# Optimization experiments

Measured on AMD Instinct MI355X. Metric: run time of the kernel, lower is better.

## Reference

```python
import jax, jax.numpy as jnp
import numpy as np

HEADS = 8

def setup_inputs() -> dict:
    key = jax.random.key(0)
    ks = jax.random.split(key, 4)
    b, n, d = 4, 4097, 128  # n = 64*64 + 1 (CLS + spatial)
    x = jax.random.normal(ks[0], (b, n, d), dtype=jnp.float32)
    W_qkv = jax.random.normal(ks[1], (d, 3 * d), dtype=jnp.float32) * (d ** -0.5)
    b_qkv = jnp.zeros((3 * d,), dtype=jnp.float32)
    W_out = jax.random.normal(ks[2], (d, d), dtype=jnp.float32) * (d ** -0.5)
    b_out = jnp.zeros((d,), dtype=jnp.float32)
    return {"x": x, "W_qkv": W_qkv, "b_qkv": b_qkv, "W_out": W_out, "b_out": b_out}

def reference(x, W_qkv, b_qkv, W_out, b_out):
    b, n, d = x.shape
    h = HEADS
    dh = d // h
    scale = d ** -0.5  # note: module scales by dim**-0.5, not head_dim**-0.5
    qkv = x @ W_qkv + b_qkv                      # [b, n, 3d]
    q, k, v = jnp.split(qkv, 3, axis=-1)
    def to_heads(t):
        return t.reshape(b, n, h, dh).transpose(0, 2, 1, 3)  # [b, h, n, dh]
    q, k, v = to_heads(q), to_heads(k), to_heads(v)
    dots = jnp.einsum('bhid,bhjd->bhij', q, k) * scale       # [b, h, n, n]
    attn = jax.nn.softmax(dots, axis=-1)
    out = jnp.einsum('bhij,bhjd->bhid', attn, v)             # [b, h, n, dh]
    out = out.transpose(0, 2, 1, 3).reshape(b, n, d)
    return out @ W_out + b_out
```

## Files before the change

### kernel.cpp

```cpp
#include <hip/hip_runtime.h>
#include <hip/hip_bf16.h>
#include <stdint.h>


#define BB 4
#define NN 4097
#define NNP 4112
#define DD 128
#define HH 8
#define DH 16
#define BH (BB*HH)
#define ROWS (BB*NN)
#define MT  1025

typedef _Float16 h4 __attribute__((ext_vector_type(4)));
typedef _Float16 h8 __attribute__((ext_vector_type(8)));
typedef __fp16   fp16v2 __attribute__((ext_vector_type(2)));
typedef float    f4 __attribute__((ext_vector_type(4)));

#define QSCALE (0.08838834764831845f * 1.4426950408889634f)

#if __has_builtin(__builtin_amdgcn_exp2f)
#define EXP2F(x) __builtin_amdgcn_exp2f(x)
#else
#define EXP2F(x) exp2f(x)
#endif

union H4u { h4 v; fp16v2 p[2]; };
union H8u { h8 v; fp16v2 p[4]; };

static __device__ __forceinline__ H4u pack4u(float a, float b, float c, float d) {
    H4u u;
#if __has_builtin(__builtin_amdgcn_cvt_pkrtz)
    u.p[0] = __builtin_amdgcn_cvt_pkrtz(a, b);
    u.p[1] = __builtin_amdgcn_cvt_pkrtz(c, d);
#else
    u.v[0] = (_Float16)a; u.v[1] = (_Float16)b; u.v[2] = (_Float16)c; u.v[3] = (_Float16)d;
#endif
    return u;
}

__global__ __launch_bounds__(256) void prep(
    const float* __restrict__ x,
    const float* __restrict__ Wqkv,
    const float* __restrict__ Wout,
    _Float16* __restrict__ x16,
    _Float16* __restrict__ WqkvT,
    _Float16* __restrict__ WoutT)
{
    const int id = blockIdx.x*256 + threadIdx.x;
    const int NX8 = ROWS*DD/8;
    if (id < NX8) {
        const float4* s = (const float4*)(x + (size_t)id*8);
        const float4 a = s[0], b = s[1];
        const H4u u0 = pack4u(a.x, a.y, a.z, a.w);
        const H4u u1 = pack4u(b.x, b.y, b.z, b.w);
        h4* d = (h4*)(x16 + (size_t)id*8);
        d[0] = u0.v; d[1] = u1.v;
    } else if (id < NX8 + 384*128) {
        const int e = id - NX8;
        const int n = e >> 7, k = e & 127;
        const float s = (n < 128) ? QSCALE : 1.0f;
        WqkvT[e] = (_Float16)(Wqkv[k*384 + n] * s);
    } else if (id < NX8 + 384*128 + 128*128) {
        const int e = id - NX8 - 384*128;
        const int n = e >> 7, k = e & 127;
        WoutT[e] = (_Float16)(Wout[k*128 + n]);
    }
}

__global__ __launch_bounds__(256) void qkv_mfma(
    const _Float16* __restrict__ x16,
    const _Float16* __restrict__ WqkvT,
    const float* __restrict__ bqkv,
    _Float16* __restrict__ Qh,
    _Float16* __restrict__ Kh,
    _Float16* __restrict__ Vh)
{
    const int wid  = blockIdx.x;
    const int wave = threadIdx.x >> 6;
    const int lane = threadIdx.x & 63;
    const int quad = lane >> 4, l16 = lane & 15;

    const int arow = wid*16 + l16;
    const int arc  = (arow < ROWS) ? arow : (ROWS - 1);
    h8 af[4];
    #pragma unroll
    for (int kk = 0; kk < 4; ++kk)
        af[kk] = *(const h8*)(x16 + (size_t)arc*DD + kk*32 + quad*8);

    const int r0 = wid*16 + quad*4;
    const int nt0 = wave*6;

    for (int nt = nt0; nt < nt0 + 6; nt += 2) {
        const float b0 = bqkv[nt*16 + l16]      * ((nt   < 8) ? QSCALE : 1.0f);
        const float b1 = bqkv[nt*16 + 16 + l16] * ((nt+1 < 8) ? QSCALE : 1.0f);
        f4 a0 = {b0,b0,b0,b0}, a1 = {b1,b1,b1,b1};
        #pragma unroll
        for (int kk = 0; kk < 4; ++kk) {
            const h8 bf0 = *(const h8*)(WqkvT + (size_t)(nt*16      + l16)*DD + kk*32 + quad*8);
            const h8 bf1 = *(const h8*)(WqkvT + (size_t)(nt*16 + 16 + l16)*DD + kk*32 + quad*8);
            a0 = __builtin_amdgcn_mfma_f32_16x16x32_f16(af[kk], bf0, a0, 0, 0, 0);
            a1 = __builtin_amdgcn_mfma_f32_16x16x32_f16(af[kk], bf1, a1, 0, 0, 0);
        }
        #pragma unroll
        for (int u = 0; u < 2; ++u) {
            const int ntc = nt + u;
            const int which = ntc >> 3, head = ntc & 7;
            _Float16* base = (which == 0) ? Qh : ((which == 1) ? Kh : Vh);
            const f4 av = u ? a1 : a0;
            #pragma unroll
            for (int r = 0; r < 4; ++r) {
                const int row = r0 + r;
                if (row < ROWS) {
                    const int bidx = row / NN;
                    const int nrow = row - bidx*NN;
                    base[((size_t)(bidx*HH + head)*NNP + nrow)*DH + l16] = (_Float16)av[r];
                }
            }
        }
    }
}

__global__ __launch_bounds__(256) void vt_transpose(
    const _Float16* __restrict__ Vh,
    _Float16* __restrict__ Vt)
{
    __shared__ _Float16 tile[128][DH + 2];
    const int tl  = blockIdx.x;
    const int bh  = blockIdx.y;
    const int tid = threadIdx.x;
    const int n0  = tl * 128;
    const int rem = (n0 + 128 <= NNP) ? 128 : (NNP - n0);

    {
        const int r  = tid >> 1;
        const int i8 = (tid & 1) * 8;
        const int rc = (r < rem) ? r : (rem - 1);
        const h8 v = *(const h8*)(Vh + ((size_t)bh*NNP + n0 + rc)*DH + i8);
        #pragma unroll
        for (int j = 0; j < 8; ++j) tile[r][i8 + j] = v[j];
    }
    __syncthreads();
    {
        const int i    = tid >> 4;
        const int nseg = tid & 15;
        if (nseg * 8 < rem) {
            h8 v;
            #pragma unroll
            for (int j = 0; j < 8; ++j) v[j] = tile[nseg*8 + j][i];
            *(h8*)(Vt + ((size_t)bh*DH + i)*NNP + n0 + nseg*8) = v;
        }
    }
}

__global__ __launch_bounds__(128, 6) void attn_mfma(
    const _Float16* __restrict__ Qh,
    const _Float16* __restrict__ Kh,
    const _Float16* __restrict__ Vt,
    _Float16* __restrict__ PACC,
    float* __restrict__ PL)
{
    const int qc2  = blockIdx.x;
    const int bh   = blockIdx.y;
    const int sp   = blockIdx.z;
    const int tid  = threadIdx.x;
    const int wave = tid >> 6;
    const int lane = tid & 63;
    const int quad = lane >> 4;
    const int l16  = lane & 15;
    const int bidx = bh >> 3, head = bh & 7;

    const int qbase = (qc2*2 + wave)*64;

    const _Float16* Qb = Qh + (size_t)bh*NNP*DH;
    h8 qf[4];
    #pragma unroll
    for (int g = 0; g < 4; ++g) {
        h8 t = {0,0,0,0,0,0,0,0};
        if (quad < 2) {
            const int qr = qbase + g*16 + l16;
            const int qc = (qr < NN) ? qr : (NN-1);
            t = *(const h8*)(Qb + (size_t)qc*DH + quad*8);
        }
        qf[g] = t;
    }

    f4 acc[4] = {{0,0,0,0},{0,0,0,0},{0,0,0,0},{0,0,0,0}};
    float ls[4] = {0.f,0.f,0.f,0.f};

    const int t0 = sp*64;
    const int t1 = t0 + 64;

    const _Float16* kp = Kh + ((size_t)bh*NNP + (size_t)t0*16 + l16)*DH + (quad&1)*8;
    const _Float16* vp = Vt + ((size_t)bh*DH + l16)*NNP + t0*16 + quad*4;

    h8 ak = *(const h8*)kp;
    h4 av = *(const h4*)vp;
    const f4 zero = {0.f,0.f,0.f,0.f};
#if __has_builtin(__builtin_amdgcn_fdot2)
    const fp16v2 one2 = {(__fp16)1.0f, (__fp16)1.0f};
#endif

    for (int tt = t0; tt < t1; ++tt) {
        kp += 16*DH; vp += 16;
        const h8 nak = *(const h8*)kp;
        const h4 nav = *(const h4*)vp;
        #pragma unroll
        for (int g = 0; g < 4; ++g) {
            f4 d = __builtin_amdgcn_mfma_f32_16x16x32_f16(ak, qf[g], zero, 0, 0, 0);
            const float p0 = EXP2F(d[0]), p1 = EXP2F(d[1]), p2 = EXP2F(d[2]), p3 = EXP2F(d[3]);
            const H4u pb = pack4u(p0, p1, p2, p3);
#if __has_builtin(__builtin_amdgcn_fdot2)
            ls[g] = __builtin_amdgcn_fdot2(pb.p[0], one2,
                     __builtin_amdgcn_fdot2(pb.p[1], one2, ls[g], false), false);
#else
            ls[g] += (p0 + p1) + (p2 + p3);
#endif
            acc[g] = __builtin_amdgcn_mfma_f32_16x16x16f16(av, pb.v, acc[g], 0, 0, 0);
        }
        ak = nak; av = nav;
    }

    if (sp == 3) {
        #pragma unroll
        for (int g = 0; g < 4; ++g) {
            f4 d = __builtin_amdgcn_mfma_f32_16x16x32_f16(ak, qf[g], zero, 0, 0, 0);
            const float p0 = (quad == 0) ? EXP2F(d[0]) : 0.f;
            ls[g] += p0;
            const H4u pb = pack4u(p0, 0.f, 0.f, 0.f);
            acc[g] = __builtin_amdgcn_mfma_f32_16x16x16f16(av, pb.v, acc[g], 0, 0, 0);
        }
    }

    const size_t rb = (size_t)sp*ROWS + (size_t)bidx*NN;
    #pragma unroll
    for (int g = 0; g < 4; ++g) {
        float l = ls[g];
        l += __shfl_xor(l, 16);
        l += __shfl_xor(l, 32);
        const int qr = qbase + g*16 + l16;
        if (qr < NN) {
            const float inv = 1.0f / l;
            const H4u st = pack4u(acc[g][0]*inv, acc[g][1]*inv, acc[g][2]*inv, acc[g][3]*inv);
            *(h4*)(PACC + (rb + qr)*DD + head*DH + quad*4) = st.v;
            if (quad == 0) PL[(rb + qr)*HH + head] = l;
        }
    }
}

__global__ __launch_bounds__(256) void out_mfma(
    const _Float16* __restrict__ PACC,
    const float* __restrict__ PL,
    const _Float16* __restrict__ WoutT,
    const float* __restrict__ bout,
    float* __restrict__ out)
{
    const int wid  = blockIdx.x*4 + (threadIdx.x >> 6);
    if (wid >= MT) return;
    const int lane = threadIdx.x & 63;
    const int quad = lane >> 4, l16 = lane & 15;
    const int hq   = quad >> 1;

    const int arow = wid*16 + l16;
    const int arc  = (arow < ROWS) ? arow : (ROWS - 1);

    h8 af[4];
    #pragma unroll
    for (int kk = 0; kk < 4; ++kk) {
        const int head = kk*2 + hq;
        float n0=0.f,n1=0.f,n2=0.f,n3=0.f,n4=0.f,n5=0.f,n6=0.f,n7=0.f,lsum=0.f;
        #pragma unroll
        for (int sp = 0; sp < 4; ++sp) {
            const float l = PL[((size_t)sp*ROWS + arc)*HH + head];
            lsum += l;
            const h8 p = *(const h8*)(PACC + ((size_t)sp*ROWS + arc)*DD + kk*32 + quad*8);
            n0 += l*(float)p[0]; n1 += l*(float)p[1];
            n2 += l*(float)p[2]; n3 += l*(float)p[3];
            n4 += l*(float)p[4]; n5 += l*(float)p[5];
            n6 += l*(float)p[6]; n7 += l*(float)p[7];
        }
        const float inv = 1.0f / lsum;
        H8u u;
#if __has_builtin(__builtin_amdgcn_cvt_pkrtz)
        u.p[0] = __builtin_amdgcn_cvt_pkrtz(n0*inv, n1*inv);
        u.p[1] = __builtin_amdgcn_cvt_pkrtz(n2*inv, n3*inv);
        u.p[2] = __builtin_amdgcn_cvt_pkrtz(n4*inv, n5*inv);
        u.p[3] = __builtin_amdgcn_cvt_pkrtz(n6*inv, n7*inv);
#else
        u.v[0]=(_Float16)(n0*inv); u.v[1]=(_Float16)(n1*inv);
        u.v[2]=(_Float16)(n2*inv); u.v[3]=(_Float16)(n3*inv);
        u.v[4]=(_Float16)(n4*inv); u.v[5]=(_Float16)(n5*inv);
        u.v[6]=(_Float16)(n6*inv); u.v[7]=(_Float16)(n7*inv);
#endif
        af[kk] = u.v;
    }

    const int r0 = wid*16 + quad*4;

    for (int nt = 0; nt < 8; nt += 2) {
        const float b0 = bout[nt*16 + l16];
        const float b1 = bout[nt*16 + 16 + l16];
        f4 a0 = {b0,b0,b0,b0}, a1 = {b1,b1,b1,b1};
        #pragma unroll
        for (int kk = 0; kk < 4; ++kk) {
            const h8 bf0 = *(const h8*)(WoutT + (size_t)(nt*16      + l16)*DD + kk*32 + quad*8);
            const h8 bf1 = *(const h8*)(WoutT + (size_t)(nt*16 + 16 + l16)*DD + kk*32 + quad*8);
            a0 = __builtin_amdgcn_mfma_f32_16x16x32_f16(af[kk], bf0, a0, 0, 0, 0);
            a1 = __builtin_amdgcn_mfma_f32_16x16x32_f16(af[kk], bf1, a1, 0, 0, 0);
        }
        #pragma unroll
        for (int r = 0; r < 4; ++r) {
            const int row = r0 + r;
            if (row < ROWS) {
                out[(size_t)row*DD + nt*16      + l16] = a0[r];
                out[(size_t)row*DD + nt*16 + 16 + l16] = a1[r];
            }
        }
    }
}

extern "C" void kernel_launch(void* const* d_in, const int* in_sizes, int n_in,
                              void* d_out, int out_size, void* d_ws, size_t ws_size,
                              hipStream_t stream) {
    const float* x    = (const float*)d_in[0];
    const float* Wqkv = (const float*)d_in[1];
    const float* bqkv = (const float*)d_in[2];
    const float* Wout = (const float*)d_in[3];
    const float* bout = (const float*)d_in[4];
    for (int i = 0; i < n_in; ++i) {
        switch (in_sizes[i]) {
            case 2097664: x    = (const float*)d_in[i]; break;
            case 49152:   Wqkv = (const float*)d_in[i]; break;
            case 384:     bqkv = (const float*)d_in[i]; break;
            case 16384:   Wout = (const float*)d_in[i]; break;
            case 128:     bout = (const float*)d_in[i]; break;
            default: break;
        }
    }
    float* out = (float*)d_out;

    const size_t perh = (size_t)BH * NNP * DH;
    _Float16* Qh   = (_Float16*)d_ws;
    _Float16* Kh   = Qh + perh;
    _Float16* Vt   = Kh + perh;
    _Float16* Vh   = Vt + perh;
    _Float16* PACC = Vh;
    _Float16* x16  = Vh + perh;
    float*    PL    = (float*)(PACC + (size_t)4*ROWS*DD);
    _Float16* WqkvT = (_Float16*)(PL + (size_t)4*ROWS*HH);
    _Float16* WoutT = WqkvT + 384*128;

    const int NX8 = ROWS*DD/8;
    const int prep_total = NX8 + 384*128 + 128*128;

    hipLaunchKernelGGL(prep, dim3((prep_total + 255)/256), dim3(256), 0, stream,
                       x, Wqkv, Wout, x16, WqkvT, WoutT);
    hipLaunchKernelGGL(qkv_mfma, dim3(MT), dim3(256), 0, stream,
                       x16, WqkvT, bqkv, Qh, Kh, Vh);
    hipLaunchKernelGGL(vt_transpose, dim3(33, BH), dim3(256), 0, stream,
                       Vh, Vt);
    hipLaunchKernelGGL(attn_mfma, dim3(33, BH, 4), dim3(128), 0, stream,
                       Qh, Kh, Vt, PACC, PL);
    hipLaunchKernelGGL(out_mfma, dim3((MT + 3)/4), dim3(256), 0, stream,
                       PACC, PL, WoutT, bout, out);
}
```

Measured before the change: 188.2 us.

## Halve KV splits, use 256-thread attention blocks with 16x16x16 QK MFMA

The attention kernel now splits the key range into two chunks instead of four and uses 256-thread blocks covering 256 query rows, with the launch grid adjusted to match. The QK product switches from a zero-padded 16x16x32 MFMA to a 16x16x16 MFMA with h4 fragments. The key loop is unrolled by two. The output kernel preloads all partial results and the whole W_out fragment set into registers before merging the two splits. The aim is to cut the partial-result write and merge traffic and remove the wasted half of the QK MFMA, at the cost of fewer total blocks for load balancing and more register pressure in out_mfma.

```diff
diff --git a/kernel.cpp b/kernel.cpp
--- a/kernel.cpp
+++ b/kernel.cpp
@@ -12,6 +12,7 @@
 #define BH (BB*HH)
 #define ROWS (BB*NN)
 #define MT  1025
+#define NSP 2
 
 typedef _Float16 h4 __attribute__((ext_vector_type(4)));
 typedef _Float16 h8 __attribute__((ext_vector_type(8)));
@@ -154,14 +155,14 @@
     }
 }
 
-__global__ __launch_bounds__(128, 6) void attn_mfma(
+__global__ __launch_bounds__(256, 8) void attn_mfma(
     const _Float16* __restrict__ Qh,
     const _Float16* __restrict__ Kh,
     const _Float16* __restrict__ Vt,
     _Float16* __restrict__ PACC,
     float* __restrict__ PL)
 {
-    const int qc2  = blockIdx.x;
+    const int qt   = blockIdx.x;
     const int bh   = blockIdx.y;
     const int sp   = blockIdx.z;
     const int tid  = threadIdx.x;
@@ -171,44 +172,41 @@
     const int l16  = lane & 15;
     const int bidx = bh >> 3, head = bh & 7;
 
-    const int qbase = (qc2*2 + wave)*64;
+    const int qbase = qt*256 + wave*64;
 
     const _Float16* Qb = Qh + (size_t)bh*NNP*DH;
-    h8 qf[4];
+    h4 qf[4];
     #pragma unroll
     for (int g = 0; g < 4; ++g) {
-        h8 t = {0,0,0,0,0,0,0,0};
-        if (quad < 2) {
-            const int qr = qbase + g*16 + l16;
-            const int qc = (qr < NN) ? qr : (NN-1);
-            t = *(const h8*)(Qb + (size_t)qc*DH + quad*8);
-        }
-        qf[g] = t;
+        const int qr = qbase + g*16 + l16;
+        const int qc = (qr < NN) ? qr : (NN-1);
+        qf[g] = *(const h4*)(Qb + (size_t)qc*DH + quad*4);
     }
 
     f4 acc[4] = {{0,0,0,0},{0,0,0,0},{0,0,0,0},{0,0,0,0}};
     float ls[4] = {0.f,0.f,0.f,0.f};
 
-    const int t0 = sp*64;
-    const int t1 = t0 + 64;
-
-    const _Float16* kp = Kh + ((size_t)bh*NNP + (size_t)t0*16 + l16)*DH + (quad&1)*8;
+    const int t0 = sp*(4096/NSP/16);
+    const int t1 = t0 + (4096/NSP/16);
+
+    const _Float16* kp = Kh + ((size_t)bh*NNP + (size_t)t0*16 + l16)*DH + quad*4;
     const _Float16* vp = Vt + ((size_t)bh*DH + l16)*NNP + t0*16 + quad*4;
 
-    h8 ak = *(const h8*)kp;
+    h4 ak = *(const h4*)kp;
     h4 av = *(const h4*)vp;
     const f4 zero = {0.f,0.f,0.f,0.f};
 #if __has_builtin(__builtin_amdgcn_fdot2)
     const fp16v2 one2 = {(__fp16)1.0f, (__fp16)1.0f};
 #endif
 
+    #pragma unroll 2
     for (int tt = t0; tt < t1; ++tt) {
         kp += 16*DH; vp += 16;
-        const h8 nak = *(const h8*)kp;
+        const h4 nak = *(const h4*)kp;
         const h4 nav = *(const h4*)vp;
         #pragma unroll
         for (int g = 0; g < 4; ++g) {
-            f4 d = __builtin_amdgcn_mfma_f32_16x16x32_f16(ak, qf[g], zero, 0, 0, 0);
+            f4 d = __builtin_amdgcn_mfma_f32_16x16x16f16(ak, qf[g], zero, 0, 0, 0);
             const float p0 = EXP2F(d[0]), p1 = EXP2F(d[1]), p2 = EXP2F(d[2]), p3 = EXP2F(d[3]);
             const H4u pb = pack4u(p0, p1, p2, p3);
 #if __has_builtin(__builtin_amdgcn_fdot2)
@@ -222,10 +220,10 @@
         ak = nak; av = nav;
     }
 
-    if (sp == 3) {
+    if (sp == NSP-1) {
         #pragma unroll
         for (int g = 0; g < 4; ++g) {
-            f4 d = __builtin_amdgcn_mfma_f32_16x16x32_f16(ak, qf[g], zero, 0, 0, 0);
+            f4 d = __builtin_amdgcn_mfma_f32_16x16x16f16(ak, qf[g], zero, 0, 0, 0);
             const float p0 = (quad == 0) ? EXP2F(d[0]) : 0.f;
             ls[g] += p0;
             const H4u pb = pack4u(p0, 0.f, 0.f, 0.f);
@@ -249,7 +247,7 @@
     }
 }
 
-__global__ __launch_bounds__(256) void out_mfma(
+__global__ __launch_bounds__(256, 1) void out_mfma(
     const _Float16* __restrict__ PACC,
     const float* __restrict__ PL,
     const _Float16* __restrict__ WoutT,
@@ -265,49 +263,58 @@
     const int arow = wid*16 + l16;
     const int arc  = (arow < ROWS) ? arow : (ROWS - 1);
 
+    h8 pf[NSP][4]; float lv[NSP][4];
+    #pragma unroll
+    for (int sp = 0; sp < NSP; ++sp) {
+        const _Float16* pb  = PACC + ((size_t)sp*ROWS + arc)*DD;
+        const float*    plb = PL   + ((size_t)sp*ROWS + arc)*HH;
+        #pragma unroll
+        for (int kk = 0; kk < 4; ++kk) {
+            pf[sp][kk] = *(const h8*)(pb + kk*32 + quad*8);
+            lv[sp][kk] = plb[kk*2 + hq];
+        }
+    }
+    h8 wf[4][2][4];
+    #pragma unroll
+    for (int p = 0; p < 4; ++p)
+        #pragma unroll
+        for (int u = 0; u < 2; ++u)
+            #pragma unroll
+            for (int kk = 0; kk < 4; ++kk)
+                wf[p][u][kk] = *(const h8*)(WoutT + (size_t)((p*2+u)*16 + l16)*DD + kk*32 + quad*8);
+
     h8 af[4];
     #pragma unroll
     for (int kk = 0; kk < 4; ++kk) {
-        const int head = kk*2 + hq;
-        float n0=0.f,n1=0.f,n2=0.f,n3=0.f,n4=0.f,n5=0.f,n6=0.f,n7=0.f,lsum=0.f;
-        #pragma unroll
-        for (int sp = 0; sp < 4; ++sp) {
-            const float l = PL[((size_t)sp*ROWS + arc)*HH + head];
-            lsum += l;
-            const h8 p = *(const h8*)(PACC + ((size_t)sp*ROWS + arc)*DD + kk*32 + quad*8);
-            n0 += l*(float)p[0]; n1 += l*(float)p[1];
-            n2 += l*(float)p[2]; n3 += l*(float)p[3];
-            n4 += l*(float)p[4]; n5 += l*(float)p[5];
-            n6 += l*(float)p[6]; n7 += l*(float)p[7];
-        }
-        const float inv = 1.0f / lsum;
+        const float l0 = lv[0][kk], l1 = lv[1][kk];
+        const float inv = 1.0f / (l0 + l1);
+        const float s0 = l0*inv, s1 = l1*inv;
         H8u u;
+        #pragma unroll
+        for (int j = 0; j < 4; ++j) {
+            const float a = s0*(float)pf[0][kk][2*j]   + s1*(float)pf[1][kk][2*j];
+            const float b = s0*(float)pf[0][kk][2*j+1] + s1*(float)pf[1][kk][2*j+1];
 #if __has_builtin(__builtin_amdgcn_cvt_pkrtz)
-        u.p[0] = __builtin_amdgcn_cvt_pkrtz(n0*inv, n1*inv);
-        u.p[1] = __builtin_amdgcn_cvt_pkrtz(n2*inv, n3*inv);
-        u.p[2] = __builtin_amdgcn_cvt_pkrtz(n4*inv, n5*inv);
-        u.p[3] = __builtin_amdgcn_cvt_pkrtz(n6*inv, n7*inv);
+            u.p[j] = __builtin_amdgcn_cvt_pkrtz(a, b);
 #else
-        u.v[0]=(_Float16)(n0*inv); u.v[1]=(_Float16)(n1*inv);
-        u.v[2]=(_Float16)(n2*inv); u.v[3]=(_Float16)(n3*inv);
-        u.v[4]=(_Float16)(n4*inv); u.v[5]=(_Float16)(n5*inv);
-        u.v[6]=(_Float16)(n6*inv); u.v[7]=(_Float16)(n7*inv);
-#endif
+            u.v[2*j] = (_Float16)a; u.v[2*j+1] = (_Float16)b;
+#endif
+        }
         af[kk] = u.v;
     }
 
     const int r0 = wid*16 + quad*4;
 
-    for (int nt = 0; nt < 8; nt += 2) {
+    #pragma unroll
+    for (int p = 0; p < 4; ++p) {
+        const int nt = p*2;
         const float b0 = bout[nt*16 + l16];
         const float b1 = bout[nt*16 + 16 + l16];
         f4 a0 = {b0,b0,b0,b0}, a1 = {b1,b1,b1,b1};
         #pragma unroll
         for (int kk = 0; kk < 4; ++kk) {
-            const h8 bf0 = *(const h8*)(WoutT + (size_t)(nt*16      + l16)*DD + kk*32 + quad*8);
-            const h8 bf1 = *(const h8*)(WoutT + (size_t)(nt*16 + 16 + l16)*DD + kk*32 + quad*8);
-            a0 = __builtin_amdgcn_mfma_f32_16x16x32_f16(af[kk], bf0, a0, 0, 0, 0);
-            a1 = __builtin_amdgcn_mfma_f32_16x16x32_f16(af[kk], bf1, a1, 0, 0, 0);
+            a0 = __builtin_amdgcn_mfma_f32_16x16x32_f16(af[kk], wf[p][0][kk], a0, 0, 0, 0);
+            a1 = __builtin_amdgcn_mfma_f32_16x16x32_f16(af[kk], wf[p][1][kk], a1, 0, 0, 0);
         }
         #pragma unroll
         for (int r = 0; r < 4; ++r) {
@@ -347,8 +354,8 @@
     _Float16* Vh   = Vt + perh;
     _Float16* PACC = Vh;
     _Float16* x16  = Vh + perh;
-    float*    PL    = (float*)(PACC + (size_t)4*ROWS*DD);
-    _Float16* WqkvT = (_Float16*)(PL + (size_t)4*ROWS*HH);
+    float*    PL    = (float*)(PACC + (size_t)NSP*ROWS*DD);
+    _Float16* WqkvT = (_Float16*)(PL + (size_t)NSP*ROWS*HH);
     _Float16* WoutT = WqkvT + 384*128;
 
     const int NX8 = ROWS*DD/8;
@@ -360,7 +367,7 @@
                        x16, WqkvT, bqkv, Qh, Kh, Vh);
     hipLaunchKernelGGL(vt_transpose, dim3(33, BH), dim3(256), 0, stream,
                        Vh, Vt);
-    hipLaunchKernelGGL(attn_mfma, dim3(33, BH, 4), dim3(128), 0, stream,
+    hipLaunchKernelGGL(attn_mfma, dim3(17, BH, NSP), dim3(256), 0, stream,
                        Qh, Kh, Vt, PACC, PL);
     hipLaunchKernelGGL(out_mfma, dim3((MT + 3)/4), dim3(256), 0, stream,
                        PACC, PL, WoutT, bout, out);
```

Result: no change. 185.3 us (-1.5%).
